# Performance work log

Measured on AMD Instinct MI355X. Metric: run time of the kernel, lower is better.

The kernel has to match this reference:

```python
import jax, jax.numpy as jnp
import numpy as np

D_IN = 1024
D_H = 1024

def setup_inputs() -> dict:
    key = jax.random.key(0)
    ks = jax.random.split(key, 9)
    s = 1.0 / np.sqrt(D_IN)
    inp = {
        'x': jax.random.normal(ks[0], (4, 2048, D_IN), dtype=jnp.float32),
        'wq': jax.random.uniform(ks[1], (D_IN, D_H), jnp.float32, -s, s),
        'bq': jax.random.uniform(ks[2], (D_H,), jnp.float32, -s, s),
        'wk': jax.random.uniform(ks[3], (D_IN, D_H), jnp.float32, -s, s),
        'bk': jax.random.uniform(ks[4], (D_H,), jnp.float32, -s, s),
        'wv': jax.random.uniform(ks[5], (D_IN, D_H), jnp.float32, -s, s),
        'bv': jax.random.uniform(ks[6], (D_H,), jnp.float32, -s, s),
        'wo': jax.random.uniform(ks[7], (D_H, D_IN), jnp.float32, -s, s),
        'bo': jax.random.uniform(ks[8], (D_IN,), jnp.float32, -s, s),
    }
    return inp

def reference(x, wq, bq, wk, bk, wv, bv, wo, bo):
    # q,k,v: [b, s, d]
    q = x @ wq + bq
    k = x @ wk + bk
    v = x @ wv + bv
    scale = 1.0 / jnp.sqrt(jnp.asarray(D_H, x.dtype))
    attn = jnp.einsum('bqd,bkd->bqk', q, k) * scale  # [b, s, s]
    attn = jax.nn.softmax(attn, axis=-1)
    score = jnp.einsum('bqk,bkd->bqd', attn, v)
    out = score @ wo + bo
    return out
```

## Files before the change

### kernel.cpp

```cpp
#include <hip/hip_runtime.h>


typedef unsigned short u16;
typedef short bf16x8 __attribute__((ext_vector_type(8)));
typedef float f32x4 __attribute__((ext_vector_type(4)));

#define SEQ 2048
#define DIM 1024

__device__ __forceinline__ u16 f2bf(float f) {
    unsigned u = __builtin_bit_cast(unsigned, f);
    u += 0x7fffu + ((u >> 16) & 1u);
    return (u16)(u >> 16);
}

__device__ __forceinline__ void async16(void* lds, const void* gmem) {
    __builtin_amdgcn_global_load_lds(
        (const __attribute__((address_space(1))) void*)gmem,
        (__attribute__((address_space(3))) void*)lds, 16, 0, 0);
}

#define FENCE() asm volatile("" ::: "memory")

__global__ __launch_bounds__(256) void cast_x_kernel(
    const float* __restrict__ x, u16* __restrict__ xb,
    const float* __restrict__ bq, const float* __restrict__ bk,
    const float* __restrict__ bv, float* __restrict__ bqkv,
    float* __restrict__ l)
{
    const int b = blockIdx.x;
    if (b < 8192) {
        const int idx = b * 256 + threadIdx.x;
        float4 v = ((const float4*)x)[idx];
        ushort4 o;
        o.x = f2bf(v.x); o.y = f2bf(v.y); o.z = f2bf(v.z); o.w = f2bf(v.w);
        ((ushort4*)xb)[idx] = o;
    } else {
        const int i = (b - 8192) * 256 + threadIdx.x;
        if (i < 3072)
            bqkv[i] = (i < 1024) ? bq[i] : (i < 2048) ? bk[i - 1024] : bv[i - 2048];
        else if (i < 3072 + 8192)
            l[i - 3072] = 0.f;
    }
}

__global__ __launch_bounds__(256) void transpose_cast_all(
    const float* __restrict__ W0, const float* __restrict__ W1,
    const float* __restrict__ W2, const float* __restrict__ W3,
    u16* __restrict__ Tqkv, u16* __restrict__ To)
{
    __shared__ float tile[32][33];
    const int z = blockIdx.z;
    const float* W = (z == 0) ? W0 : (z == 1) ? W1 : (z == 2) ? W2 : W3;
    u16* T = (z < 3) ? (Tqkv + (size_t)z * 1048576) : To;

    const int bx = blockIdx.x * 32, by = blockIdx.y * 32;
    const int tx = threadIdx.x, ty = threadIdx.y;
    #pragma unroll
    for (int r = 0; r < 4; ++r)
        tile[ty + r * 8][tx] = W[(size_t)(by + ty + r * 8) * DIM + bx + tx];
    __syncthreads();
    #pragma unroll
    for (int r = 0; r < 4; ++r) {
        const float v = tile[tx][ty + r * 8];
        T[(size_t)(bx + ty + r * 8) * DIM + by + tx] = f2bf(v);
    }
}

#define EPI_BF16BIAS 0
#define EPI_BF16     1
#define EPI_ELOGIT   2
#define EPI_PVOUT    3

template<int EPI, int K, int LDA, int LDB, int LDC>
__global__ __launch_bounds__(256, 2) void gemm4w(
    const u16* __restrict__ A, const u16* __restrict__ Bt,
    const float* __restrict__ bias, u16* __restrict__ C,
    float* __restrict__ Cf, float* __restrict__ lsum,
    float scale, long sA, long sB, long sC)
{
    __shared__ u16 lds[2][2][8192];

    constexpr int NT = K / 64;

    const int z = blockIdx.z;
    const int t = threadIdx.x;
    const int wid = t >> 6, lane = t & 63;
    const int wm = wid >> 1, wn = wid & 1;
    const int lrow = lane & 15, quad = lane >> 4;
    const int m0 = blockIdx.y * 128, n0 = blockIdx.x * 128;

    const u16* ABase = A  + (size_t)z * sA + (size_t)m0 * LDA;
    const u16* BBase = Bt + (size_t)z * sB + (size_t)n0 * LDB;

    int srow[4], scolOff[4];
    #pragma unroll
    for (int p = 0; p < 4; ++p) {
        const int slot = p * 256 + t;
        const int row  = slot >> 3;
        const int c8   = (slot & 7) ^ (row & 7);
        srow[p] = row; scolOff[p] = c8 * 8;
    }

    auto stage = [&](int tile, int buf) {
        const int k0 = tile * 64;
        #pragma unroll
        for (int p = 0; p < 4; ++p) {
            const int slot = p * 256 + t;
            async16(&lds[buf][0][slot * 8],
                    ABase + (size_t)srow[p] * LDA + k0 + scolOff[p]);
        }
        #pragma unroll
        for (int p = 0; p < 4; ++p) {
            const int slot = p * 256 + t;
            async16(&lds[buf][1][slot * 8],
                    BBase + (size_t)srow[p] * LDB + k0 + scolOff[p]);
        }
    };

    f32x4 acc[4][4];
    #pragma unroll
    for (int i = 0; i < 4; ++i)
        #pragma unroll
        for (int j = 0; j < 4; ++j)
            acc[i][j] = (f32x4){0.f, 0.f, 0.f, 0.f};

    auto ldA1 = [&](int buf, int mi, int ks) -> bf16x8 {
        int b = (wm * 64 + mi * 16 + lrow) * 128 + ks * 64 + quad * 16;
        b ^= ((b >> 7) & 7) << 4;
        return *(const bf16x8*)((const char*)&lds[buf][0][0] + b);
    };
    auto ldB1 = [&](int buf, int ni, int ks) -> bf16x8 {
        int b = (wn * 64 + ni * 16 + lrow) * 128 + ks * 64 + quad * 16;
        b ^= ((b >> 7) & 7) << 4;
        return *(const bf16x8*)((const char*)&lds[buf][1][0] + b);
    };

    stage(0, 0);
    stage(1, 1);

    #pragma unroll 1
    for (int T = 0; T < NT; ++T) {
        const int buf = T & 1;
        if (T + 1 < NT) asm volatile("s_waitcnt vmcnt(8)" ::: "memory");
        else            asm volatile("s_waitcnt vmcnt(0)" ::: "memory");
        __builtin_amdgcn_s_barrier();

        #pragma unroll
        for (int ks = 0; ks < 2; ++ks) {
            bf16x8 aF[4], bF[4];
            #pragma unroll
            for (int mi = 0; mi < 4; ++mi) aF[mi] = ldA1(buf, mi, ks);
            #pragma unroll
            for (int ni = 0; ni < 4; ++ni) bF[ni] = ldB1(buf, ni, ks);
            __builtin_amdgcn_s_setprio(1);
            #pragma unroll
            for (int mi = 0; mi < 4; ++mi)
                #pragma unroll
                for (int ni = 0; ni < 4; ++ni)
                    acc[mi][ni] = __builtin_amdgcn_mfma_f32_16x16x32_bf16(
                        aF[mi], bF[ni], acc[mi][ni], 0, 0, 0);
            __builtin_amdgcn_s_setprio(0);
        }
        FENCE();
        __builtin_amdgcn_s_barrier();
        if (T + 2 < NT) stage(T + 2, buf);
    }

    u16*   Cz  = C  + (size_t)z * sC;
    float* Cfz = Cf ? Cf + (size_t)z * sC : nullptr;

    #pragma unroll
    for (int mi = 0; mi < 4; ++mi) {
        const int row = m0 + wm * 64 + mi * 16 + quad * 4;
        if (EPI == EPI_BF16BIAS) {
            #pragma unroll
            for (int ni = 0; ni < 4; ++ni) {
                const int col = n0 + wn * 64 + ni * 16 + lrow;
                const float bb = bias[col];
                const f32x4 a = acc[mi][ni];
                #pragma unroll
                for (int r = 0; r < 4; ++r)
                    Cz[(size_t)(row + r) * LDC + col] = f2bf(a[r] + bb);
            }
        } else if (EPI == EPI_BF16) {
            #pragma unroll
            for (int ni = 0; ni < 4; ++ni) {
                const int col = n0 + wn * 64 + ni * 16 + lrow;
                const f32x4 a = acc[mi][ni];
                #pragma unroll
                for (int r = 0; r < 4; ++r)
                    Cz[(size_t)(row + r) * LDC + col] = f2bf(a[r]);
            }
        } else if (EPI == EPI_ELOGIT) {
            float rs[4] = {0.f, 0.f, 0.f, 0.f};
            #pragma unroll
            for (int ni = 0; ni < 4; ++ni) {
                const int col = n0 + wn * 64 + ni * 16 + lrow;
                const f32x4 a = acc[mi][ni];
                #pragma unroll
                for (int r = 0; r < 4; ++r) {
                    const float e = __expf(a[r] * scale);
                    Cz[(size_t)(row + r) * LDC + col] = f2bf(e);
                    rs[r] += e;
                }
            }
            #pragma unroll
            for (int r = 0; r < 4; ++r) {
                float s = rs[r];
                s += __shfl_xor(s, 1, 64);
                s += __shfl_xor(s, 2, 64);
                s += __shfl_xor(s, 4, 64);
                s += __shfl_xor(s, 8, 64);
                if (lrow == 0)
                    atomicAdd(&lsum[(size_t)z * 2048 + row + r], s);
            }
        } else {
            float linv[4];
            #pragma unroll
            for (int r = 0; r < 4; ++r)
                linv[r] = 1.0f / lsum[(size_t)z * 2048 + row + r];
            #pragma unroll
            for (int ni = 0; ni < 4; ++ni) {
                const int col = n0 + wn * 64 + ni * 16 + lrow;
                const float bb = bias[col];
                const f32x4 a = acc[mi][ni];
                #pragma unroll
                for (int r = 0; r < 4; ++r)
                    Cfz[(size_t)(row + r) * LDC + col] = a[r] * linv[r] + bb;
            }
        }
    }
}

extern "C" void kernel_launch(void* const* d_in, const int* in_sizes, int n_in,
                              void* d_out, int out_size, void* d_ws, size_t ws_size,
                              hipStream_t stream)
{
    const float* x  = (const float*)d_in[0];
    const float* wq = (const float*)d_in[1];
    const float* bq = (const float*)d_in[2];
    const float* wk = (const float*)d_in[3];
    const float* bk = (const float*)d_in[4];
    const float* wv = (const float*)d_in[5];
    const float* bv = (const float*)d_in[6];
    const float* wo = (const float*)d_in[7];
    const float* bo = (const float*)d_in[8];
    float* out = (float*)d_out;

    u16* w16   = (u16*)d_ws;
    u16* xb    = w16;
    u16* qkv   = w16 + 8388608;
    u16* E     = w16 + 33554432;
    u16* wqkvT = w16 + 50331648;
    u16* woT   = w16 + 53477376;
    float* bqkv = (float*)(w16 + 54525952);
    float* l    = (float*)(w16 + 54532096);
    u16* VWoT  = w16;

    const u16* q_ = qkv;
    const u16* k_ = qkv + 1024;
    const u16* v_ = qkv + 2048;

    cast_x_kernel<<<8236, dim3(256), 0, stream>>>(x, xb, bq, bk, bv, bqkv, l);
    transpose_cast_all<<<dim3(32, 32, 4), dim3(32, 8), 0, stream>>>(
        wq, wk, wv, wo, wqkvT, woT);

    gemm4w<EPI_BF16BIAS, 1024, 1024, 1024, 3072>
        <<<dim3(24, 64, 1), dim3(256), 0, stream>>>(
            xb, wqkvT, bqkv, qkv, nullptr, nullptr, 1.f, 0, 0, 0);

    gemm4w<EPI_ELOGIT, 1024, 3072, 3072, 2048>
        <<<dim3(16, 16, 4), dim3(256), 0, stream>>>(
            q_, k_, nullptr, E, nullptr, l, 0.03125f,
            6291456, 6291456, 4194304);

    gemm4w<EPI_BF16, 1024, 1024, 3072, 2048>
        <<<dim3(16, 8, 4), dim3(256), 0, stream>>>(
            woT, v_, nullptr, VWoT, nullptr, nullptr, 1.f,
            0, 6291456, 2097152);

    gemm4w<EPI_PVOUT, 2048, 2048, 2048, 1024>
        <<<dim3(8, 16, 4), dim3(256), 0, stream>>>(
            E, VWoT, bo, nullptr, out, l, 1.f,
            4194304, 2097152, 2097152);
}
```

Measured before the change: 273.9 us.

## Add single-buffered 256x128 GEMM kernel with staggered block start for three GEMMs

Adds a new GEMM kernel, gemmW, with a 256x128 output tile per block and 8x4 MFMA fragments per wave. It uses single-buffered LDS with a wait and barrier on every k-tile, and targets 3 blocks per CU. Blocks stagger their start with s_sleep based on block index, to spread out the initial memory bursts. The QKV, logits and V·Wo GEMMs move to this kernel with halved grid heights, while the PV/out GEMM stays on gemm4w, whose epilogue is trimmed to the two paths still used and which now also sleeps on odd blocks. The larger tile raises reuse per loaded byte, but dropping double buffering exposes load latency unless occupancy hides it, and the bigger accumulator array raises register pressure.

After: 799.6 us. +191.9%, slower.

```diff
diff --git a/kernel.cpp b/kernel.cpp
--- a/kernel.cpp
+++ b/kernel.cpp
@@ -73,6 +73,161 @@
 #define EPI_PVOUT    3
 
 template<int EPI, int K, int LDA, int LDB, int LDC>
+__global__ __launch_bounds__(256, 3) void gemmW(
+    const u16* __restrict__ A, const u16* __restrict__ Bt,
+    const float* __restrict__ bias, u16* __restrict__ C,
+    float* __restrict__ Cf, float* __restrict__ lsum,
+    float scale, long sA, long sB, long sC)
+{
+    __shared__ u16 sAt[256 * 64];
+    __shared__ u16 sBt[128 * 64];
+
+    constexpr int NT = K / 64;
+
+    const int z = blockIdx.z;
+    const int t = threadIdx.x;
+    const int wid = t >> 6, lane = t & 63;
+    const int wm = wid >> 1, wn = wid & 1;
+    const int lrow = lane & 15, quad = lane >> 4;
+    const int m0 = blockIdx.y * 256, n0 = blockIdx.x * 128;
+
+    const int lin = blockIdx.x + gridDim.x * (blockIdx.y + gridDim.y * z);
+    const int slot = lin % 3;
+    if (slot > 0) __builtin_amdgcn_s_sleep(8);
+    if (slot > 1) __builtin_amdgcn_s_sleep(8);
+
+    const u16* ABase = A  + (size_t)z * sA + (size_t)m0 * LDA;
+    const u16* BBase = Bt + (size_t)z * sB + (size_t)n0 * LDB;
+
+    int offA[8], offB[4];
+    #pragma unroll
+    for (int p = 0; p < 8; ++p) {
+        const int s = p * 256 + t, row = s >> 3, c8 = (s & 7) ^ (row & 7);
+        offA[p] = row * LDA + c8 * 8;
+    }
+    #pragma unroll
+    for (int p = 0; p < 4; ++p) {
+        const int s = p * 256 + t, row = s >> 3, c8 = (s & 7) ^ (row & 7);
+        offB[p] = row * LDB + c8 * 8;
+    }
+
+    f32x4 acc[8][4];
+    #pragma unroll
+    for (int i = 0; i < 8; ++i)
+        #pragma unroll
+        for (int j = 0; j < 4; ++j)
+            acc[i][j] = (f32x4){0.f, 0.f, 0.f, 0.f};
+
+    auto ldA1 = [&](int mi, int ks) -> bf16x8 {
+        int b = (wm * 128 + mi * 16 + lrow) * 128 + ks * 64 + quad * 16;
+        b ^= ((b >> 7) & 7) << 4;
+        return *(const bf16x8*)((const char*)sAt + b);
+    };
+    auto ldB1 = [&](int ni, int ks) -> bf16x8 {
+        int b = (wn * 64 + ni * 16 + lrow) * 128 + ks * 64 + quad * 16;
+        b ^= ((b >> 7) & 7) << 4;
+        return *(const bf16x8*)((const char*)sBt + b);
+    };
+
+    #pragma unroll 1
+    for (int T = 0; T < NT; ++T) {
+        const int k0 = T * 64;
+        #pragma unroll
+        for (int p = 0; p < 8; ++p)
+            async16(&sAt[(p * 256 + t) * 8], ABase + k0 + offA[p]);
+        #pragma unroll
+        for (int p = 0; p < 4; ++p)
+            async16(&sBt[(p * 256 + t) * 8], BBase + k0 + offB[p]);
+        asm volatile("s_waitcnt vmcnt(0)" ::: "memory");
+        __builtin_amdgcn_s_barrier();
+
+        #pragma unroll
+        for (int ks = 0; ks < 2; ++ks) {
+            bf16x8 aF[8], bF[4];
+            #pragma unroll
+            for (int mi = 0; mi < 8; ++mi) aF[mi] = ldA1(mi, ks);
+            #pragma unroll
+            for (int ni = 0; ni < 4; ++ni) bF[ni] = ldB1(ni, ks);
+            __builtin_amdgcn_s_setprio(1);
+            #pragma unroll
+            for (int mi = 0; mi < 8; ++mi)
+                #pragma unroll
+                for (int ni = 0; ni < 4; ++ni)
+                    acc[mi][ni] = __builtin_amdgcn_mfma_f32_16x16x32_bf16(
+                        aF[mi], bF[ni], acc[mi][ni], 0, 0, 0);
+            __builtin_amdgcn_s_setprio(0);
+        }
+        FENCE();
+        __builtin_amdgcn_s_barrier();
+    }
+
+    u16*   Cz  = C  + (size_t)z * sC;
+    float* Cfz = Cf ? Cf + (size_t)z * sC : nullptr;
+
+    #pragma unroll
+    for (int mi = 0; mi < 8; ++mi) {
+        const int row = m0 + wm * 128 + mi * 16 + quad * 4;
+        if (EPI == EPI_BF16BIAS) {
+            #pragma unroll
+            for (int ni = 0; ni < 4; ++ni) {
+                const int col = n0 + wn * 64 + ni * 16 + lrow;
+                const float bb = bias[col];
+                const f32x4 a = acc[mi][ni];
+                #pragma unroll
+                for (int r = 0; r < 4; ++r)
+                    Cz[(size_t)(row + r) * LDC + col] = f2bf(a[r] + bb);
+            }
+        } else if (EPI == EPI_BF16) {
+            #pragma unroll
+            for (int ni = 0; ni < 4; ++ni) {
+                const int col = n0 + wn * 64 + ni * 16 + lrow;
+                const f32x4 a = acc[mi][ni];
+                #pragma unroll
+                for (int r = 0; r < 4; ++r)
+                    Cz[(size_t)(row + r) * LDC + col] = f2bf(a[r]);
+            }
+        } else if (EPI == EPI_ELOGIT) {
+            float rs[4] = {0.f, 0.f, 0.f, 0.f};
+            #pragma unroll
+            for (int ni = 0; ni < 4; ++ni) {
+                const int col = n0 + wn * 64 + ni * 16 + lrow;
+                const f32x4 a = acc[mi][ni];
+                #pragma unroll
+                for (int r = 0; r < 4; ++r) {
+                    const float e = __expf(a[r] * scale);
+                    Cz[(size_t)(row + r) * LDC + col] = f2bf(e);
+                    rs[r] += e;
+                }
+            }
+            #pragma unroll
+            for (int r = 0; r < 4; ++r) {
+                float s = rs[r];
+                s += __shfl_xor(s, 1, 64);
+                s += __shfl_xor(s, 2, 64);
+                s += __shfl_xor(s, 4, 64);
+                s += __shfl_xor(s, 8, 64);
+                if (lrow == 0)
+                    atomicAdd(&lsum[(size_t)z * 2048 + row + r], s);
+            }
+        } else {
+            float linv[4];
+            #pragma unroll
+            for (int r = 0; r < 4; ++r)
+                linv[r] = 1.0f / lsum[(size_t)z * 2048 + row + r];
+            #pragma unroll
+            for (int ni = 0; ni < 4; ++ni) {
+                const int col = n0 + wn * 64 + ni * 16 + lrow;
+                const float bb = bias[col];
+                const f32x4 a = acc[mi][ni];
+                #pragma unroll
+                for (int r = 0; r < 4; ++r)
+                    Cfz[(size_t)(row + r) * LDC + col] = a[r] * linv[r] + bb;
+            }
+        }
+    }
+}
+
+template<int EPI, int K, int LDA, int LDB, int LDC>
 __global__ __launch_bounds__(256, 2) void gemm4w(
     const u16* __restrict__ A, const u16* __restrict__ Bt,
     const float* __restrict__ bias, u16* __restrict__ C,
@@ -90,15 +245,16 @@
     const int lrow = lane & 15, quad = lane >> 4;
     const int m0 = blockIdx.y * 128, n0 = blockIdx.x * 128;
 
+    const int lin = blockIdx.x + gridDim.x * (blockIdx.y + gridDim.y * z);
+    if (lin & 1) __builtin_amdgcn_s_sleep(8);
+
     const u16* ABase = A  + (size_t)z * sA + (size_t)m0 * LDA;
     const u16* BBase = Bt + (size_t)z * sB + (size_t)n0 * LDB;
 
     int srow[4], scolOff[4];
     #pragma unroll
     for (int p = 0; p < 4; ++p) {
-        const int slot = p * 256 + t;
-        const int row  = slot >> 3;
-        const int c8   = (slot & 7) ^ (row & 7);
+        const int s = p * 256 + t, row = s >> 3, c8 = (s & 7) ^ (row & 7);
         srow[p] = row; scolOff[p] = c8 * 8;
     }
 
@@ -106,14 +262,14 @@
         const int k0 = tile * 64;
         #pragma unroll
         for (int p = 0; p < 4; ++p) {
-            const int slot = p * 256 + t;
-            async16(&lds[buf][0][slot * 8],
+            const int s = p * 256 + t;
+            async16(&lds[buf][0][s * 8],
                     ABase + (size_t)srow[p] * LDA + k0 + scolOff[p]);
         }
         #pragma unroll
         for (int p = 0; p < 4; ++p) {
-            const int slot = p * 256 + t;
-            async16(&lds[buf][1][slot * 8],
+            const int s = p * 256 + t;
+            async16(&lds[buf][1][s * 8],
                     BBase + (size_t)srow[p] * LDB + k0 + scolOff[p]);
         }
     };
@@ -173,7 +329,11 @@
     #pragma unroll
     for (int mi = 0; mi < 4; ++mi) {
         const int row = m0 + wm * 64 + mi * 16 + quad * 4;
-        if (EPI == EPI_BF16BIAS) {
+        if (EPI == EPI_PVOUT) {
+            float linv[4];
+            #pragma unroll
+            for (int r = 0; r < 4; ++r)
+                linv[r] = 1.0f / lsum[(size_t)z * 2048 + row + r];
             #pragma unroll
             for (int ni = 0; ni < 4; ++ni) {
                 const int col = n0 + wn * 64 + ni * 16 + lrow;
@@ -181,9 +341,9 @@
                 const f32x4 a = acc[mi][ni];
                 #pragma unroll
                 for (int r = 0; r < 4; ++r)
-                    Cz[(size_t)(row + r) * LDC + col] = f2bf(a[r] + bb);
-            }
-        } else if (EPI == EPI_BF16) {
+                    Cfz[(size_t)(row + r) * LDC + col] = a[r] * linv[r] + bb;
+            }
+        } else {
             #pragma unroll
             for (int ni = 0; ni < 4; ++ni) {
                 const int col = n0 + wn * 64 + ni * 16 + lrow;
@@ -191,43 +351,6 @@
                 #pragma unroll
                 for (int r = 0; r < 4; ++r)
                     Cz[(size_t)(row + r) * LDC + col] = f2bf(a[r]);
-            }
-        } else if (EPI == EPI_ELOGIT) {
-            float rs[4] = {0.f, 0.f, 0.f, 0.f};
-            #pragma unroll
-            for (int ni = 0; ni < 4; ++ni) {
-                const int col = n0 + wn * 64 + ni * 16 + lrow;
-                const f32x4 a = acc[mi][ni];
-                #pragma unroll
-                for (int r = 0; r < 4; ++r) {
-                    const float e = __expf(a[r] * scale);
-                    Cz[(size_t)(row + r) * LDC + col] = f2bf(e);
-                    rs[r] += e;
-                }
-            }
-            #pragma unroll
-            for (int r = 0; r < 4; ++r) {
-                float s = rs[r];
-                s += __shfl_xor(s, 1, 64);
-                s += __shfl_xor(s, 2, 64);
-                s += __shfl_xor(s, 4, 64);
-                s += __shfl_xor(s, 8, 64);
-                if (lrow == 0)
-                    atomicAdd(&lsum[(size_t)z * 2048 + row + r], s);
-            }
-        } else {
-            float linv[4];
-            #pragma unroll
-            for (int r = 0; r < 4; ++r)
-                linv[r] = 1.0f / lsum[(size_t)z * 2048 + row + r];
-            #pragma unroll
-            for (int ni = 0; ni < 4; ++ni) {
-                const int col = n0 + wn * 64 + ni * 16 + lrow;
-                const float bb = bias[col];
-                const f32x4 a = acc[mi][ni];
-                #pragma unroll
-                for (int r = 0; r < 4; ++r)
-                    Cfz[(size_t)(row + r) * LDC + col] = a[r] * linv[r] + bb;
             }
         }
     }
@@ -266,17 +389,17 @@
     transpose_cast_all<<<dim3(32, 32, 4), dim3(32, 8), 0, stream>>>(
         wq, wk, wv, wo, wqkvT, woT);
 
-    gemm4w<EPI_BF16BIAS, 1024, 1024, 1024, 3072>
-        <<<dim3(24, 64, 1), dim3(256), 0, stream>>>(
+    gemmW<EPI_BF16BIAS, 1024, 1024, 1024, 3072>
+        <<<dim3(24, 32, 1), dim3(256), 0, stream>>>(
             xb, wqkvT, bqkv, qkv, nullptr, nullptr, 1.f, 0, 0, 0);
 
-    gemm4w<EPI_ELOGIT, 1024, 3072, 3072, 2048>
-        <<<dim3(16, 16, 4), dim3(256), 0, stream>>>(
+    gemmW<EPI_ELOGIT, 1024, 3072, 3072, 2048>
+        <<<dim3(16, 8, 4), dim3(256), 0, stream>>>(
             q_, k_, nullptr, E, nullptr, l, 0.03125f,
             6291456, 6291456, 4194304);
 
-    gemm4w<EPI_BF16, 1024, 1024, 3072, 2048>
-        <<<dim3(16, 8, 4), dim3(256), 0, stream>>>(
+    gemmW<EPI_BF16, 1024, 1024, 3072, 2048>
+        <<<dim3(16, 4, 4), dim3(256), 0, stream>>>(
             woT, v_, nullptr, VWoT, nullptr, nullptr, 1.f,
             0, 6291456, 2097152);
 
```

## Prefetch next tile's LDS fragments into registers while issuing current MFMAs

Applied to the files above, without the earlier changes.

Restructures the GEMM main loop into a register double-buffered pipeline: fragments for tile T+1 are read from LDS into a second register set before the MFMAs for tile T are issued, and the loop is unrolled by two to alternate the register sets. The aim is to hide LDS read latency behind MFMA execution. In exchange it waits for all outstanding global loads (vmcnt(0)) each step, which may expose global load latency, and it doubles fragment register usage, which could hurt occupancy under launch_bounds(256,2).

Result: slower. 308.5 us (+12.6%).

```diff
diff --git a/kernel.cpp b/kernel.cpp
--- a/kernel.cpp
+++ b/kernel.cpp
@@ -82,6 +82,7 @@
     __shared__ u16 lds[2][2][8192];
 
     constexpr int NT = K / 64;
+    static_assert(NT % 2 == 0 && NT >= 4, "NT even");
 
     const int z = blockIdx.z;
     const int t = threadIdx.x;
@@ -96,9 +97,7 @@
     int srow[4], scolOff[4];
     #pragma unroll
     for (int p = 0; p < 4; ++p) {
-        const int slot = p * 256 + t;
-        const int row  = slot >> 3;
-        const int c8   = (slot & 7) ^ (row & 7);
+        const int s = p * 256 + t, row = s >> 3, c8 = (s & 7) ^ (row & 7);
         srow[p] = row; scolOff[p] = c8 * 8;
     }
 
@@ -106,14 +105,14 @@
         const int k0 = tile * 64;
         #pragma unroll
         for (int p = 0; p < 4; ++p) {
-            const int slot = p * 256 + t;
-            async16(&lds[buf][0][slot * 8],
+            const int s = p * 256 + t;
+            async16(&lds[buf][0][s * 8],
                     ABase + (size_t)srow[p] * LDA + k0 + scolOff[p]);
         }
         #pragma unroll
         for (int p = 0; p < 4; ++p) {
-            const int slot = p * 256 + t;
-            async16(&lds[buf][1][slot * 8],
+            const int s = p * 256 + t;
+            async16(&lds[buf][1][s * 8],
                     BBase + (size_t)srow[p] * LDB + k0 + scolOff[p]);
         }
     };
@@ -136,35 +135,53 @@
         return *(const bf16x8*)((const char*)&lds[buf][1][0] + b);
     };
 
+    bf16x8 a0[4][2], b0[4][2], a1[4][2], b1[4][2];
+
+    auto readFrags = [&](int buf, bf16x8 (&aF)[4][2], bf16x8 (&bF)[4][2]) {
+        #pragma unroll
+        for (int ks = 0; ks < 2; ++ks) {
+            #pragma unroll
+            for (int mi = 0; mi < 4; ++mi) aF[mi][ks] = ldA1(buf, mi, ks);
+            #pragma unroll
+            for (int ni = 0; ni < 4; ++ni) bF[ni][ks] = ldB1(buf, ni, ks);
+        }
+    };
+    auto mfmaAll = [&](bf16x8 (&aF)[4][2], bf16x8 (&bF)[4][2]) {
+        __builtin_amdgcn_s_setprio(1);
+        #pragma unroll
+        for (int ks = 0; ks < 2; ++ks)
+            #pragma unroll
+            for (int mi = 0; mi < 4; ++mi)
+                #pragma unroll
+                for (int ni = 0; ni < 4; ++ni)
+                    acc[mi][ni] = __builtin_amdgcn_mfma_f32_16x16x32_bf16(
+                        aF[mi][ks], bF[ni][ks], acc[mi][ni], 0, 0, 0);
+        __builtin_amdgcn_s_setprio(0);
+    };
+
+    auto step = [&](int T, bf16x8 (&cA)[4][2], bf16x8 (&cB)[4][2],
+                           bf16x8 (&nA)[4][2], bf16x8 (&nB)[4][2]) {
+        if (T + 1 < NT) {
+            asm volatile("s_waitcnt vmcnt(0)" ::: "memory");
+            __builtin_amdgcn_s_barrier();
+            readFrags((T + 1) & 1, nA, nB);
+        }
+        mfmaAll(cA, cB);
+        FENCE();
+        __builtin_amdgcn_s_barrier();
+        if (T + 2 < NT) stage(T + 2, T & 1);
+    };
+
     stage(0, 0);
     stage(1, 1);
+    asm volatile("s_waitcnt vmcnt(8)" ::: "memory");
+    __builtin_amdgcn_s_barrier();
+    readFrags(0, a0, b0);
 
     #pragma unroll 1
-    for (int T = 0; T < NT; ++T) {
-        const int buf = T & 1;
-        if (T + 1 < NT) asm volatile("s_waitcnt vmcnt(8)" ::: "memory");
-        else            asm volatile("s_waitcnt vmcnt(0)" ::: "memory");
-        __builtin_amdgcn_s_barrier();
-
-        #pragma unroll
-        for (int ks = 0; ks < 2; ++ks) {
-            bf16x8 aF[4], bF[4];
-            #pragma unroll
-            for (int mi = 0; mi < 4; ++mi) aF[mi] = ldA1(buf, mi, ks);
-            #pragma unroll
-            for (int ni = 0; ni < 4; ++ni) bF[ni] = ldB1(buf, ni, ks);
-            __builtin_amdgcn_s_setprio(1);
-            #pragma unroll
-            for (int mi = 0; mi < 4; ++mi)
-                #pragma unroll
-                for (int ni = 0; ni < 4; ++ni)
-                    acc[mi][ni] = __builtin_amdgcn_mfma_f32_16x16x32_bf16(
-                        aF[mi], bF[ni], acc[mi][ni], 0, 0, 0);
-            __builtin_amdgcn_s_setprio(0);
-        }
-        FENCE();
-        __builtin_amdgcn_s_barrier();
-        if (T + 2 < NT) stage(T + 2, buf);
+    for (int T = 0; T < NT; T += 2) {
+        step(T,     a0, b0, a1, b1);
+        step(T + 1, a1, b1, a0, b0);
     }
 
     u16*   Cz  = C  + (size_t)z * sC;
```

## Use two-wave 128x128 GEMM blocks with 64x128 per-wave tiles and K-step 32

Applied to the files above, without the earlier changes.

Rewrites the shared GEMM kernel so that each 128x128 output tile is handled by two waves instead of four. Each wave now computes a 64x128 sub-tile with 32 accumulators, and the K tile shrinks from 64 to 32. The aim is to raise per-wave register reuse of A and B fragments and to halve the LDS footprint, allowing more blocks per CU. In exchange there are twice as many barriers per unit of K, fewer waves per block to hide latency, and higher register pressure that may cause spills under launch_bounds(128,2).

Measured after the change: 294.7 us. +7.6%, slower.

```diff
diff --git a/kernel.cpp b/kernel.cpp
--- a/kernel.cpp
+++ b/kernel.cpp
@@ -73,66 +73,61 @@
 #define EPI_PVOUT    3
 
 template<int EPI, int K, int LDA, int LDB, int LDC>
-__global__ __launch_bounds__(256, 2) void gemm4w(
+__global__ __launch_bounds__(128, 2) void gemm2x(
     const u16* __restrict__ A, const u16* __restrict__ Bt,
     const float* __restrict__ bias, u16* __restrict__ C,
     float* __restrict__ Cf, float* __restrict__ lsum,
     float scale, long sA, long sB, long sC)
 {
-    __shared__ u16 lds[2][2][8192];
-
-    constexpr int NT = K / 64;
+    __shared__ u16 lds[2][2][4096];
+
+    constexpr int NT = K / 32;
+    static_assert(NT >= 4, "K >= 128");
 
     const int z = blockIdx.z;
     const int t = threadIdx.x;
-    const int wid = t >> 6, lane = t & 63;
-    const int wm = wid >> 1, wn = wid & 1;
+    const int w = t >> 6, lane = t & 63;
     const int lrow = lane & 15, quad = lane >> 4;
     const int m0 = blockIdx.y * 128, n0 = blockIdx.x * 128;
 
     const u16* ABase = A  + (size_t)z * sA + (size_t)m0 * LDA;
     const u16* BBase = Bt + (size_t)z * sB + (size_t)n0 * LDB;
 
-    int srow[4], scolOff[4];
+    int offA[4], offB[4];
     #pragma unroll
     for (int p = 0; p < 4; ++p) {
-        const int slot = p * 256 + t;
-        const int row  = slot >> 3;
-        const int c8   = (slot & 7) ^ (row & 7);
-        srow[p] = row; scolOff[p] = c8 * 8;
+        const int s = p * 128 + t;
+        const int row = s >> 2;
+        const int c4 = (s & 3) ^ ((row >> 1) & 3);
+        offA[p] = row * LDA + c4 * 8;
+        offB[p] = row * LDB + c4 * 8;
     }
 
     auto stage = [&](int tile, int buf) {
-        const int k0 = tile * 64;
-        #pragma unroll
-        for (int p = 0; p < 4; ++p) {
-            const int slot = p * 256 + t;
-            async16(&lds[buf][0][slot * 8],
-                    ABase + (size_t)srow[p] * LDA + k0 + scolOff[p]);
-        }
-        #pragma unroll
-        for (int p = 0; p < 4; ++p) {
-            const int slot = p * 256 + t;
-            async16(&lds[buf][1][slot * 8],
-                    BBase + (size_t)srow[p] * LDB + k0 + scolOff[p]);
-        }
+        const int k0 = tile * 32;
+        #pragma unroll
+        for (int p = 0; p < 4; ++p)
+            async16(&lds[buf][0][(p * 128 + t) * 8], ABase + k0 + offA[p]);
+        #pragma unroll
+        for (int p = 0; p < 4; ++p)
+            async16(&lds[buf][1][(p * 128 + t) * 8], BBase + k0 + offB[p]);
     };
 
-    f32x4 acc[4][4];
+    f32x4 acc[4][8];
     #pragma unroll
     for (int i = 0; i < 4; ++i)
         #pragma unroll
-        for (int j = 0; j < 4; ++j)
+        for (int j = 0; j < 8; ++j)
             acc[i][j] = (f32x4){0.f, 0.f, 0.f, 0.f};
 
-    auto ldA1 = [&](int buf, int mi, int ks) -> bf16x8 {
-        int b = (wm * 64 + mi * 16 + lrow) * 128 + ks * 64 + quad * 16;
-        b ^= ((b >> 7) & 7) << 4;
+    auto ldA1 = [&](int buf, int mi) -> bf16x8 {
+        int b = (w * 64 + mi * 16 + lrow) * 64 + quad * 16;
+        b ^= ((b >> 7) & 3) << 4;
         return *(const bf16x8*)((const char*)&lds[buf][0][0] + b);
     };
-    auto ldB1 = [&](int buf, int ni, int ks) -> bf16x8 {
-        int b = (wn * 64 + ni * 16 + lrow) * 128 + ks * 64 + quad * 16;
-        b ^= ((b >> 7) & 7) << 4;
+    auto ldB1 = [&](int buf, int ni) -> bf16x8 {
+        int b = (ni * 16 + lrow) * 64 + quad * 16;
+        b ^= ((b >> 7) & 3) << 4;
         return *(const bf16x8*)((const char*)&lds[buf][1][0] + b);
     };
 
@@ -146,22 +141,20 @@
         else            asm volatile("s_waitcnt vmcnt(0)" ::: "memory");
         __builtin_amdgcn_s_barrier();
 
-        #pragma unroll
-        for (int ks = 0; ks < 2; ++ks) {
-            bf16x8 aF[4], bF[4];
-            #pragma unroll
-            for (int mi = 0; mi < 4; ++mi) aF[mi] = ldA1(buf, mi, ks);
-            #pragma unroll
-            for (int ni = 0; ni < 4; ++ni) bF[ni] = ldB1(buf, ni, ks);
-            __builtin_amdgcn_s_setprio(1);
-            #pragma unroll
-            for (int mi = 0; mi < 4; ++mi)
-                #pragma unroll
-                for (int ni = 0; ni < 4; ++ni)
-                    acc[mi][ni] = __builtin_amdgcn_mfma_f32_16x16x32_bf16(
-                        aF[mi], bF[ni], acc[mi][ni], 0, 0, 0);
-            __builtin_amdgcn_s_setprio(0);
-        }
+        bf16x8 aF[4], bF[8];
+        #pragma unroll
+        for (int mi = 0; mi < 4; ++mi) aF[mi] = ldA1(buf, mi);
+        #pragma unroll
+        for (int ni = 0; ni < 8; ++ni) bF[ni] = ldB1(buf, ni);
+        __builtin_amdgcn_s_setprio(1);
+        #pragma unroll
+        for (int mi = 0; mi < 4; ++mi)
+            #pragma unroll
+            for (int ni = 0; ni < 8; ++ni)
+                acc[mi][ni] = __builtin_amdgcn_mfma_f32_16x16x32_bf16(
+                    aF[mi], bF[ni], acc[mi][ni], 0, 0, 0);
+        __builtin_amdgcn_s_setprio(0);
+
         FENCE();
         __builtin_amdgcn_s_barrier();
         if (T + 2 < NT) stage(T + 2, buf);
@@ -172,11 +165,11 @@
 
     #pragma unroll
     for (int mi = 0; mi < 4; ++mi) {
-        const int row = m0 + wm * 64 + mi * 16 + quad * 4;
+        const int row = m0 + w * 64 + mi * 16 + quad * 4;
         if (EPI == EPI_BF16BIAS) {
             #pragma unroll
-            for (int ni = 0; ni < 4; ++ni) {
-                const int col = n0 + wn * 64 + ni * 16 + lrow;
+            for (int ni = 0; ni < 8; ++ni) {
+                const int col = n0 + ni * 16 + lrow;
                 const float bb = bias[col];
                 const f32x4 a = acc[mi][ni];
                 #pragma unroll
@@ -185,8 +178,8 @@
             }
         } else if (EPI == EPI_BF16) {
             #pragma unroll
-            for (int ni = 0; ni < 4; ++ni) {
-                const int col = n0 + wn * 64 + ni * 16 + lrow;
+            for (int ni = 0; ni < 8; ++ni) {
+                const int col = n0 + ni * 16 + lrow;
                 const f32x4 a = acc[mi][ni];
                 #pragma unroll
                 for (int r = 0; r < 4; ++r)
@@ -195,8 +188,8 @@
         } else if (EPI == EPI_ELOGIT) {
             float rs[4] = {0.f, 0.f, 0.f, 0.f};
             #pragma unroll
-            for (int ni = 0; ni < 4; ++ni) {
-                const int col = n0 + wn * 64 + ni * 16 + lrow;
+            for (int ni = 0; ni < 8; ++ni) {
+                const int col = n0 + ni * 16 + lrow;
                 const f32x4 a = acc[mi][ni];
                 #pragma unroll
                 for (int r = 0; r < 4; ++r) {
@@ -221,8 +214,8 @@
             for (int r = 0; r < 4; ++r)
                 linv[r] = 1.0f / lsum[(size_t)z * 2048 + row + r];
             #pragma unroll
-            for (int ni = 0; ni < 4; ++ni) {
-                const int col = n0 + wn * 64 + ni * 16 + lrow;
+            for (int ni = 0; ni < 8; ++ni) {
+                const int col = n0 + ni * 16 + lrow;
                 const float bb = bias[col];
                 const f32x4 a = acc[mi][ni];
                 #pragma unroll
@@ -266,22 +259,22 @@
     transpose_cast_all<<<dim3(32, 32, 4), dim3(32, 8), 0, stream>>>(
         wq, wk, wv, wo, wqkvT, woT);
 
-    gemm4w<EPI_BF16BIAS, 1024, 1024, 1024, 3072>
-        <<<dim3(24, 64, 1), dim3(256), 0, stream>>>(
+    gemm2x<EPI_BF16BIAS, 1024, 1024, 1024, 3072>
+        <<<dim3(24, 64, 1), dim3(128), 0, stream>>>(
             xb, wqkvT, bqkv, qkv, nullptr, nullptr, 1.f, 0, 0, 0);
 
-    gemm4w<EPI_ELOGIT, 1024, 3072, 3072, 2048>
-        <<<dim3(16, 16, 4), dim3(256), 0, stream>>>(
+    gemm2x<EPI_ELOGIT, 1024, 3072, 3072, 2048>
+        <<<dim3(16, 16, 4), dim3(128), 0, stream>>>(
             q_, k_, nullptr, E, nullptr, l, 0.03125f,
             6291456, 6291456, 4194304);
 
-    gemm4w<EPI_BF16, 1024, 1024, 3072, 2048>
-        <<<dim3(16, 8, 4), dim3(256), 0, stream>>>(
+    gemm2x<EPI_BF16, 1024, 1024, 3072, 2048>
+        <<<dim3(16, 8, 4), dim3(128), 0, stream>>>(
             woT, v_, nullptr, VWoT, nullptr, nullptr, 1.f,
             0, 6291456, 2097152);
 
-    gemm4w<EPI_PVOUT, 2048, 2048, 2048, 1024>
-        <<<dim3(8, 16, 4), dim3(256), 0, stream>>>(
+    gemm2x<EPI_PVOUT, 2048, 2048, 2048, 1024>
+        <<<dim3(8, 16, 4), dim3(128), 0, stream>>>(
             E, VWoT, bo, nullptr, out, l, 1.f,
             4194304, 2097152, 2097152);
 }
```
